# Performance work log

Hardware: AMD Instinct MI355X
Metric: run time of the kernel (lower is better)

## Reference

```python
import jax, jax.numpy as jnp
import numpy as np

B, D, O, E, H, K = 4096, 1024, 1024, 8, 4096, 2


def setup_inputs() -> dict:
    key = jax.random.key(0)
    ks = jax.random.split(key, 5)
    scale_g = 1.0 / np.sqrt(D)
    scale_1 = 1.0 / np.sqrt(D)
    scale_2 = 1.0 / np.sqrt(H)
    return {
        "x": jax.random.normal(ks[0], (B, D), jnp.float32),
        "gate_w": jax.random.normal(ks[1], (D, E), jnp.float32) * scale_g,
        "gate_b": jnp.zeros((E,), jnp.float32),
        "w1": jax.random.normal(ks[2], (E, D, H), jnp.float32) * scale_1,
        "b1": jnp.zeros((E, H), jnp.float32),
        "w2": jax.random.normal(ks[3], (E, H, O), jnp.float32) * scale_2,
        "b2": jnp.zeros((E, O), jnp.float32),
    }


def reference(x, gate_w, gate_b, w1, b1, w2, b2):
    # Router: top-k logits, softmax over the k selected logits only
    logits = x @ gate_w + gate_b                      # [B, E]
    top_vals, top_idx = jax.lax.top_k(logits, K)      # [B, K]
    routing_w = jax.nn.softmax(top_vals, axis=-1)     # [B, K]

    # Dense all-expert MLP (grouped GEMM), then gather the k selected outputs
    h = jax.nn.relu(jnp.einsum("bd,edh->beh", x, w1) + b1)  # [B, E, H]
    y = jnp.einsum("beh,eho->beo", h, w2) + b2              # [B, E, O]
    sel = jnp.take_along_axis(y, top_idx[:, :, None], axis=1)  # [B, K, O]
    return jnp.sum(routing_w[:, :, None] * sel, axis=1)        # [B, O]
```

## Files before the change

### kernel.cpp

```cpp
#include <hip/hip_runtime.h>
#include <stdint.h>

typedef short bf16x8 __attribute__((ext_vector_type(8)));
typedef float f32x4  __attribute__((ext_vector_type(4)));

constexpr int BT = 4096;
constexpr int DD = 1024;
constexpr int OO = 1024;
constexpr int EE = 8;
constexpr int HH = 4096;
constexpr int SLOTS = 2 * BT;

constexpr int BM = 128, BN = 128, BK = 32;
constexpr int A_USH = BM * BK;
constexpr int SLOT_USH = (BM + BN) * BK;
constexpr int MAXT = 72;
constexpr int G1_BLKS = 32 * MAXT;
constexpr int G2_BLKS = 8 * MAXT * 2;

__device__ __forceinline__ unsigned short f2bf(float f) {
  unsigned u = __float_as_uint(f);
  u += 0x7fffu + ((u >> 16) & 1u);
  return (unsigned short)(u >> 16);
}

__device__ __forceinline__ void glds16(const unsigned short* g, unsigned short* l) {
  __builtin_amdgcn_global_load_lds(
      (const __attribute__((address_space(1))) void*)g,
      (__attribute__((address_space(3))) void*)l, 16, 0, 0);
}

__device__ __forceinline__ void cvt_body(const float* __restrict__ src,
                                         unsigned short* __restrict__ dst,
                                         int R, int C, int e, int r0, int c0, int t,
                                         unsigned short (*tile)[66]) {
  const float* s = src + (size_t)e * R * C;
  unsigned short* d = dst + (size_t)e * R * C;
#pragma unroll
  for (int p = 0; p < 4; ++p) {
    int ch = p * 256 + t;
    int rr = ch >> 4, cc = (ch & 15) << 2;
    float4 v = *(const float4*)&s[(size_t)(r0 + rr) * C + c0 + cc];
    unsigned lo = (unsigned)f2bf(v.x) | ((unsigned)f2bf(v.y) << 16);
    unsigned hi = (unsigned)f2bf(v.z) | ((unsigned)f2bf(v.w) << 16);
    *(uint2*)&tile[rr][cc] = make_uint2(lo, hi);
  }
  __syncthreads();
#pragma unroll
  for (int p = 0; p < 4; ++p) {
    int ch = p * 256 + t;
    int cc = ch >> 4, rr = (ch & 15) << 2;
    unsigned short v0 = tile[rr + 0][cc];
    unsigned short v1 = tile[rr + 1][cc];
    unsigned short v2 = tile[rr + 2][cc];
    unsigned short v3 = tile[rr + 3][cc];
    unsigned lo = (unsigned)v0 | ((unsigned)v1 << 16);
    unsigned hi = (unsigned)v2 | ((unsigned)v3 << 16);
    *(uint2*)&d[(size_t)(c0 + cc) * R + r0 + rr] = make_uint2(lo, hi);
  }
}

__global__ __launch_bounds__(256) void fusedA_k(const float* __restrict__ x,
                                                const float* __restrict__ gw,
                                                const float* __restrict__ gb,
                                                const float* __restrict__ w1,
                                                unsigned short* __restrict__ xb,
                                                int* __restrict__ cnt,
                                                int* __restrict__ list,
                                                float* __restrict__ rw,
                                                unsigned short* __restrict__ w1t) {
  __shared__ unsigned short tile[64][66];
  int bid = blockIdx.x;
  if (bid >= 1024) {
    int idx = bid - 1024;
    int e = idx >> 10, rem = idx & 1023;
    int r0 = (rem & 15) << 6, c0 = (rem >> 4) << 6;
    cvt_body(w1, w1t, DD, HH, e, r0, c0, threadIdx.x, tile);
    return;
  }
  int wave = threadIdx.x >> 6, lane = threadIdx.x & 63;
  int b = bid * 4 + wave;
  const float* xrow = x + (size_t)b * DD;
  float acc[8];
#pragma unroll
  for (int e = 0; e < 8; ++e) acc[e] = 0.f;
#pragma unroll
  for (int i = 0; i < 4; ++i) {
    int d0 = i * 256 + lane * 4;
    float4 v = *(const float4*)&xrow[d0];
    unsigned lo = (unsigned)f2bf(v.x) | ((unsigned)f2bf(v.y) << 16);
    unsigned hi = (unsigned)f2bf(v.z) | ((unsigned)f2bf(v.w) << 16);
    *(uint2*)&xb[(size_t)b * DD + d0] = make_uint2(lo, hi);
    const float* g0 = &gw[(size_t)d0 * 8];
    float fv[4] = {v.x, v.y, v.z, v.w};
#pragma unroll
    for (int q = 0; q < 4; ++q) {
      float4 ga = *(const float4*)&g0[q * 8];
      float4 gc = *(const float4*)&g0[q * 8 + 4];
      acc[0] += fv[q] * ga.x; acc[1] += fv[q] * ga.y;
      acc[2] += fv[q] * ga.z; acc[3] += fv[q] * ga.w;
      acc[4] += fv[q] * gc.x; acc[5] += fv[q] * gc.y;
      acc[6] += fv[q] * gc.z; acc[7] += fv[q] * gc.w;
    }
  }
#pragma unroll
  for (int off = 32; off > 0; off >>= 1) {
#pragma unroll
    for (int e = 0; e < 8; ++e) acc[e] += __shfl_down(acc[e], off);
  }
  if (lane == 0) {
    float v[8];
#pragma unroll
    for (int e = 0; e < 8; ++e) v[e] = acc[e] + gb[e];
    int i0 = 0;
#pragma unroll
    for (int e = 1; e < 8; ++e) if (v[e] > v[i0]) i0 = e;
    int i1 = (i0 == 0) ? 1 : 0;
#pragma unroll
    for (int e = 0; e < 8; ++e) if (e != i0 && v[e] > v[i1]) i1 = e;
    float e1 = __expf(v[i1] - v[i0]);
    float inv = 1.0f / (1.0f + e1);
    int p0 = atomicAdd(&cnt[i0], 1);
    list[i0 * BT + p0] = 2 * b;     rw[2 * b]     = inv;
    int p1 = atomicAdd(&cnt[i1], 1);
    list[i1 * BT + p1] = 2 * b + 1; rw[2 * b + 1] = e1 * inv;
  }
}

__global__ void tilemap_k(const int* __restrict__ cnt, int* __restrict__ tmap,
                          int* __restrict__ ntiles) {
  if (threadIdx.x == 0 && blockIdx.x == 0) {
    int t = 0, basewalk = 0;
    for (int e = 0; e < EE; ++e) {
      int c = cnt[e];
      for (int m0 = 0; m0 < c; m0 += BM) {
        tmap[4 * t] = e; tmap[4 * t + 1] = m0; tmap[4 * t + 2] = basewalk + m0; ++t;
      }
      basewalk += c;
    }
    *ntiles = t;
  }
}

__global__ __launch_bounds__(256) void cvt_t_k(const float* __restrict__ src,
                                               unsigned short* __restrict__ dst,
                                               int R, int C) {
  __shared__ unsigned short tile[64][66];
  cvt_body(src, dst, R, C, blockIdx.z, blockIdx.x << 6, blockIdx.y << 6,
           threadIdx.x, tile);
}

__global__ __launch_bounds__(256, 3) void fusedB_k(const unsigned short* __restrict__ xb,
                                                   const unsigned short* __restrict__ w1t,
                                                   const float* __restrict__ b1,
                                                   const int* __restrict__ cnt,
                                                   const int* __restrict__ list,
                                                   const int* __restrict__ tmap,
                                                   const int* __restrict__ ntiles,
                                                   unsigned short* __restrict__ hc,
                                                   const float* __restrict__ w2,
                                                   unsigned short* __restrict__ w2t) {
  __shared__ __align__(16) unsigned short lds[3 * SLOT_USH];
  __shared__ int slotbuf[BM];
  int bid = blockIdx.x;
  if (bid >= G1_BLKS) {
    int idx = bid - G1_BLKS;
    int e = idx >> 10, rem = idx & 1023;
    int r0 = (rem & 63) << 6, c0 = (rem >> 6) << 6;
    cvt_body(w2, w2t, HH, OO, e, r0, c0, threadIdx.x,
             (unsigned short (*)[66])lds);
    return;
  }
  int q = bid & 7, kk = bid >> 3;
  int n0 = (kk & 31) * BN;
  int ti = (kk >> 5) * 8 + q;
  if (ti >= *ntiles) return;
  int e = tmap[4 * ti], m0 = tmap[4 * ti + 1], base = tmap[4 * ti + 2];
  int cnt_e = cnt[e];

  int t = threadIdx.x;
  if (t < BM) {
    int r = m0 + t;
    slotbuf[t] = list[e * BT + (r < cnt_e ? r : 0)];
  }
  __syncthreads();

  int w = t >> 6, l = t & 63, lm = l & 15, lq = l >> 4;
  int wm = (w >> 1) * 64, wn = (w & 1) * 64;

  const unsigned short* aS[2];
  const unsigned short* bS[2];
  int dA[2], dB[2];
#pragma unroll
  for (int j = 0; j < 2; ++j) {
    int row = w * 32 + j * 16 + (l >> 2);
    int sch = ((l & 3) ^ ((row >> 1) & 3)) * 8;
    aS[j] = xb + (size_t)(slotbuf[row] >> 1) * DD + sch;
    bS[j] = w1t + (size_t)e * HH * DD + (size_t)(n0 + row) * DD + sch;
    dA[j] = w * 1024 + j * 512;
    dB[j] = A_USH + w * 1024 + j * 512;
  }

  int xs = (lq ^ ((lm >> 1) & 3)) * 8;
  int afo[4], bfo[4];
#pragma unroll
  for (int mi = 0; mi < 4; ++mi) afo[mi] = (wm + mi * 16 + lm) * BK + xs;
#pragma unroll
  for (int ni = 0; ni < 4; ++ni) bfo[ni] = A_USH + (wn + ni * 16 + lm) * BK + xs;

  f32x4 acc[4][4];
#pragma unroll
  for (int mi = 0; mi < 4; ++mi)
#pragma unroll
    for (int ni = 0; ni < 4; ++ni) acc[mi][ni] = f32x4{0.f, 0.f, 0.f, 0.f};

  constexpr int NT = DD / BK;

#pragma unroll
  for (int p = 0; p < 2; ++p) {
    unsigned short* Lb = lds + p * SLOT_USH;
    glds16(aS[0] + p * BK, Lb + dA[0]);
    glds16(aS[1] + p * BK, Lb + dA[1]);
    glds16(bS[0] + p * BK, Lb + dB[0]);
    glds16(bS[1] + p * BK, Lb + dB[1]);
  }
  asm volatile("s_waitcnt vmcnt(4)" ::: "memory");
  __builtin_amdgcn_s_barrier();
  asm volatile("" ::: "memory");

  int sc = 0, ss = 2;
  for (int tt = 0; tt < NT; ++tt) {
    {
      int ts = tt + 2;
      int ko = (ts < NT ? ts : NT - 1) * BK;
      unsigned short* Lb = lds + ss * SLOT_USH;
      glds16(aS[0] + ko, Lb + dA[0]);
      glds16(aS[1] + ko, Lb + dA[1]);
      glds16(bS[0] + ko, Lb + dB[0]);
      glds16(bS[1] + ko, Lb + dB[1]);
    }
    const unsigned short* Lc = lds + sc * SLOT_USH;
    bf16x8 af[4], bf[4];
#pragma unroll
    for (int mi = 0; mi < 4; ++mi) af[mi] = *(const bf16x8*)&Lc[afo[mi]];
#pragma unroll
    for (int ni = 0; ni < 4; ++ni) bf[ni] = *(const bf16x8*)&Lc[bfo[ni]];
    __builtin_amdgcn_s_setprio(1);
#pragma unroll
    for (int mi = 0; mi < 4; ++mi)
#pragma unroll
      for (int ni = 0; ni < 4; ++ni)
        acc[mi][ni] = __builtin_amdgcn_mfma_f32_16x16x32_bf16(af[mi], bf[ni], acc[mi][ni], 0, 0, 0);
    __builtin_amdgcn_s_setprio(0);
    asm volatile("s_waitcnt vmcnt(4)" ::: "memory");
    __builtin_amdgcn_s_barrier();
    asm volatile("" ::: "memory");
    if (++sc == 3) sc = 0;
    if (++ss == 3) ss = 0;
  }

  asm volatile("s_waitcnt vmcnt(0)" ::: "memory");
  __builtin_amdgcn_s_barrier();
  asm volatile("" ::: "memory");
  unsigned short* cb = lds + w * 4096;
  float bias[4];
#pragma unroll
  for (int ni = 0; ni < 4; ++ni) bias[ni] = b1[e * HH + n0 + wn + ni * 16 + lm];
#pragma unroll
  for (int mi = 0; mi < 4; ++mi)
#pragma unroll
    for (int ni = 0; ni < 4; ++ni)
#pragma unroll
      for (int r = 0; r < 4; ++r)
        cb[(mi * 16 + lq * 4 + r) * 64 + ni * 16 + lm] =
            f2bf(fmaxf(acc[mi][ni][r] + bias[ni], 0.0f));
  asm volatile("s_waitcnt lgkmcnt(0)" ::: "memory");
#pragma unroll
  for (int it = 0; it < 8; ++it) {
    int rr = it * 8 + (l >> 3), chk = l & 7;
    int grow = wm + rr;
    if (m0 + grow < cnt_e) {
      uint4 v = *(const uint4*)&cb[rr * 64 + chk * 8];
      *(uint4*)&hc[(size_t)(base + grow) * HH + n0 + wn + chk * 8] = v;
    }
  }
}

__global__ __launch_bounds__(256, 3) void gemm2_k(const unsigned short* __restrict__ hc,
                                                  const unsigned short* __restrict__ w2t,
                                                  const float* __restrict__ b2,
                                                  const int* __restrict__ cnt,
                                                  const int* __restrict__ list,
                                                  const int* __restrict__ tmap,
                                                  const int* __restrict__ ntiles,
                                                  const float* __restrict__ rw,
                                                  float* __restrict__ ybuf,
                                                  float* __restrict__ out) {
  int q = blockIdx.x & 7, kk = blockIdx.x >> 3;
  int n0 = (kk & 7) * BN;
  int mz = (kk >> 3) * 8 + q;
  int z = mz / MAXT;
  int ti = mz % MAXT;
  if (ti >= *ntiles) return;
  int e = tmap[4 * ti], m0 = tmap[4 * ti + 1], base = tmap[4 * ti + 2];
  int cnt_e = cnt[e];
  int kb0 = z * (HH / 2);
  constexpr int NT = (HH / 2) / BK;

  __shared__ __align__(16) unsigned short lds[3 * SLOT_USH];
  __shared__ int slotbuf[BM];
  __shared__ float rwbuf[BM];

  int t = threadIdx.x;
  if (t < BM) {
    int r = m0 + t;
    int s_ = list[e * BT + (r < cnt_e ? r : 0)];
    slotbuf[t] = s_;
    rwbuf[t] = rw[s_];
  }
  __syncthreads();

  int w = t >> 6, l = t & 63, lm = l & 15, lq = l >> 4;
  int wm = (w >> 1) * 64, wn = (w & 1) * 64;

  const unsigned short* aS[2];
  const unsigned short* bS[2];
  int dA[2], dB[2];
#pragma unroll
  for (int j = 0; j < 2; ++j) {
    int row = w * 32 + j * 16 + (l >> 2);
    int sch = ((l & 3) ^ ((row >> 1) & 3)) * 8;
    int gr = base + row; if (gr > SLOTS - 1) gr = SLOTS - 1;
    aS[j] = hc + (size_t)gr * HH + kb0 + sch;
    bS[j] = w2t + (size_t)e * OO * HH + (size_t)(n0 + row) * HH + kb0 + sch;
    dA[j] = w * 1024 + j * 512;
    dB[j] = A_USH + w * 1024 + j * 512;
  }

  int xs = (lq ^ ((lm >> 1) & 3)) * 8;
  int afo[4], bfo[4];
#pragma unroll
  for (int mi = 0; mi < 4; ++mi) afo[mi] = (wm + mi * 16 + lm) * BK + xs;
#pragma unroll
  for (int ni = 0; ni < 4; ++ni) bfo[ni] = A_USH + (wn + ni * 16 + lm) * BK + xs;

  f32x4 acc[4][4];
#pragma unroll
  for (int mi = 0; mi < 4; ++mi)
#pragma unroll
    for (int ni = 0; ni < 4; ++ni) acc[mi][ni] = f32x4{0.f, 0.f, 0.f, 0.f};

#pragma unroll
  for (int p = 0; p < 2; ++p) {
    unsigned short* Lb = lds + p * SLOT_USH;
    glds16(aS[0] + p * BK, Lb + dA[0]);
    glds16(aS[1] + p * BK, Lb + dA[1]);
    glds16(bS[0] + p * BK, Lb + dB[0]);
    glds16(bS[1] + p * BK, Lb + dB[1]);
  }
  asm volatile("s_waitcnt vmcnt(4)" ::: "memory");
  __builtin_amdgcn_s_barrier();
  asm volatile("" ::: "memory");

  int sc = 0, ss = 2;
  for (int tt = 0; tt < NT; ++tt) {
    {
      int ts = tt + 2;
      int ko = (ts < NT ? ts : NT - 1) * BK;
      unsigned short* Lb = lds + ss * SLOT_USH;
      glds16(aS[0] + ko, Lb + dA[0]);
      glds16(aS[1] + ko, Lb + dA[1]);
      glds16(bS[0] + ko, Lb + dB[0]);
      glds16(bS[1] + ko, Lb + dB[1]);
    }
    const unsigned short* Lc = lds + sc * SLOT_USH;
    bf16x8 af[4], bf[4];
#pragma unroll
    for (int mi = 0; mi < 4; ++mi) af[mi] = *(const bf16x8*)&Lc[afo[mi]];
#pragma unroll
    for (int ni = 0; ni < 4; ++ni) bf[ni] = *(const bf16x8*)&Lc[bfo[ni]];
    __builtin_amdgcn_s_setprio(1);
#pragma unroll
    for (int mi = 0; mi < 4; ++mi)
#pragma unroll
      for (int ni = 0; ni < 4; ++ni)
        acc[mi][ni] = __builtin_amdgcn_mfma_f32_16x16x32_bf16(af[mi], bf[ni], acc[mi][ni], 0, 0, 0);
    __builtin_amdgcn_s_setprio(0);
    asm volatile("s_waitcnt vmcnt(4)" ::: "memory");
    __builtin_amdgcn_s_barrier();
    asm volatile("" ::: "memory");
    if (++sc == 3) sc = 0;
    if (++ss == 3) ss = 0;
  }
  asm volatile("s_waitcnt vmcnt(0)" ::: "memory");

  bool addb = (z == 0);
  size_t ybase = (size_t)z * SLOTS;
#pragma unroll
  for (int ni = 0; ni < 4; ++ni) {
    int ncol = n0 + wn + ni * 16 + lm;
    float bias = addb ? b2[e * OO + ncol] : 0.0f;
#pragma unroll
    for (int mi = 0; mi < 4; ++mi)
#pragma unroll
      for (int r = 0; r < 4; ++r) {
        int lrow = wm + mi * 16 + lq * 4 + r;
        if (m0 + lrow < cnt_e) {
          float v = (acc[mi][ni][r] + bias) * rwbuf[lrow];
          int slot = slotbuf[lrow];
          if (ybuf) ybuf[(ybase + slot) * OO + ncol] = v;
          else      atomicAdd(&out[(size_t)(slot >> 1) * OO + ncol], v);
        }
      }
  }
}

__global__ __launch_bounds__(256) void combine_k(const float* __restrict__ y,
                                                 float* __restrict__ out, int nz) {
  int i = blockIdx.x * 256 + threadIdx.x;
  int b = i >> 8, c = i & 255;
  f32x4 acc = {0.f, 0.f, 0.f, 0.f};
  for (int z = 0; z < nz; ++z) {
#pragma unroll
    for (int k = 0; k < 2; ++k) {
      const float4 v = *(const float4*)&y[((size_t)z * SLOTS + 2 * b + k) * OO + c * 4];
      acc[0] += v.x; acc[1] += v.y; acc[2] += v.z; acc[3] += v.w;
    }
  }
  *(f32x4*)&out[(size_t)b * OO + c * 4] = acc;
}

extern "C" void kernel_launch(void* const* d_in, const int* in_sizes, int n_in,
                              void* d_out, int out_size, void* d_ws, size_t ws_size,
                              hipStream_t stream) {
  const float* x  = (const float*)d_in[0];
  const float* gw = (const float*)d_in[1];
  const float* gb = (const float*)d_in[2];
  const float* w1 = (const float*)d_in[3];
  const float* b1 = (const float*)d_in[4];
  const float* w2 = (const float*)d_in[5];
  const float* b2 = (const float*)d_in[6];
  float* out = (float*)d_out;
  char* ws = (char*)d_ws;

  int*            cnt    = (int*)(ws);
  int*            ntiles = (int*)(ws + 64);
  int*            tmap   = (int*)(ws + 128);
  float*          rw     = (float*)(ws + 4096);
  int*            list   = (int*)(ws + (64u << 10));
  unsigned short* xb     = (unsigned short*)(ws + (1u  << 20));
  unsigned short* w1t    = (unsigned short*)(ws + (9u  << 20));

  bool roomy = ws_size >= (201u << 20);
  hipMemsetAsync(cnt, 0, 64, stream);

  if (roomy) {
    unsigned short* w2t = (unsigned short*)(ws + (73u  << 20));
    unsigned short* hc  = (unsigned short*)(ws + (137u << 20));
    float*          ybuf = (float*)(ws + (9u << 20));

    fusedA_k<<<1024 + 8192, 256, 0, stream>>>(x, gw, gb, w1, xb, cnt, list, rw, w1t);
    tilemap_k<<<1, 64, 0, stream>>>(cnt, tmap, ntiles);
    fusedB_k<<<G1_BLKS + 8192, 256, 0, stream>>>(xb, w1t, b1, cnt, list, tmap, ntiles,
                                                 hc, w2, w2t);
    gemm2_k<<<G2_BLKS, 256, 0, stream>>>(hc, w2t, b2, cnt, list, tmap,
                                         ntiles, rw, ybuf, out);
    combine_k<<<BT * OO / 1024, 256, 0, stream>>>(ybuf, out, 2);
  } else {
    if (ws_size < (137u << 20)) return;
    unsigned short* w2t = w1t;
    unsigned short* hc  = (unsigned short*)(ws + (73u << 20));
    hipMemsetAsync(out, 0, (size_t)BT * OO * sizeof(float), stream);
    fusedA_k<<<1024 + 8192, 256, 0, stream>>>(x, gw, gb, w1, xb, cnt, list, rw, w1t);
    tilemap_k<<<1, 64, 0, stream>>>(cnt, tmap, ntiles);
    fusedB_k<<<G1_BLKS, 256, 0, stream>>>(xb, w1t, b1, cnt, list, tmap, ntiles,
                                          hc, w2, w2t);
    cvt_t_k<<<dim3(HH / 64, OO / 64, EE), 256, 0, stream>>>(w2, w2t, HH, OO);
    gemm2_k<<<G2_BLKS, 256, 0, stream>>>(hc, w2t, b2, cnt, list, tmap,
                                         ntiles, rw, nullptr, out);
  }
}
```

Baseline: 654.6 us.

## Pin each expert's tiles to one XCD via per-expert tile start offsets

Both grouped GEMM kernels now map blockIdx low bits to the expert index, using per-expert tile start offsets written by tilemap_k. Before, tiles were laid out linearly across all experts. Because blocks are dispatched round-robin across XCDs, each XCD should mostly stream a single expert's weights, which is meant to improve L2 reuse of w1t and w2t. The grid is sized for the worst case of 32 tiles per expert, so many blocks exit at once. It also risks XCD load imbalance when routing is skewed toward some experts.

```diff
diff --git a/kernel.cpp b/kernel.cpp
--- a/kernel.cpp
+++ b/kernel.cpp
@@ -14,9 +14,9 @@
 constexpr int BM = 128, BN = 128, BK = 32;
 constexpr int A_USH = BM * BK;
 constexpr int SLOT_USH = (BM + BN) * BK;
-constexpr int MAXT = 72;
-constexpr int G1_BLKS = 32 * MAXT;
-constexpr int G2_BLKS = 8 * MAXT * 2;
+constexpr int MTS = 32;
+constexpr int G1_BLKS = 8 * 32 * MTS;
+constexpr int G2_BLKS = 8 * 2 * 8 * MTS;
 
 __device__ __forceinline__ unsigned short f2bf(float f) {
   unsigned u = __float_as_uint(f);
@@ -128,16 +128,18 @@
 }
 
 __global__ void tilemap_k(const int* __restrict__ cnt, int* __restrict__ tmap,
-                          int* __restrict__ ntiles) {
+                          int* __restrict__ ntiles, int* __restrict__ tstart) {
   if (threadIdx.x == 0 && blockIdx.x == 0) {
     int t = 0, basewalk = 0;
     for (int e = 0; e < EE; ++e) {
+      tstart[e] = t;
       int c = cnt[e];
       for (int m0 = 0; m0 < c; m0 += BM) {
         tmap[4 * t] = e; tmap[4 * t + 1] = m0; tmap[4 * t + 2] = basewalk + m0; ++t;
       }
       basewalk += c;
     }
+    tstart[EE] = t;
     *ntiles = t;
   }
 }
@@ -156,7 +158,7 @@
                                                    const int* __restrict__ cnt,
                                                    const int* __restrict__ list,
                                                    const int* __restrict__ tmap,
-                                                   const int* __restrict__ ntiles,
+                                                   const int* __restrict__ tstart,
                                                    unsigned short* __restrict__ hc,
                                                    const float* __restrict__ w2,
                                                    unsigned short* __restrict__ w2t) {
@@ -171,17 +173,19 @@
              (unsigned short (*)[66])lds);
     return;
   }
-  int q = bid & 7, kk = bid >> 3;
-  int n0 = (kk & 31) * BN;
-  int ti = (kk >> 5) * 8 + q;
-  if (ti >= *ntiles) return;
+  int q = bid & 7, r = bid >> 3;
+  int mts = r & (MTS - 1), nt = r >> 5;
+  int tc0 = tstart[q];
+  if (tc0 + mts >= tstart[q + 1]) return;
+  int ti = tc0 + mts;
   int e = tmap[4 * ti], m0 = tmap[4 * ti + 1], base = tmap[4 * ti + 2];
   int cnt_e = cnt[e];
+  int n0 = nt * BN;
 
   int t = threadIdx.x;
   if (t < BM) {
-    int r = m0 + t;
-    slotbuf[t] = list[e * BT + (r < cnt_e ? r : 0)];
+    int rr = m0 + t;
+    slotbuf[t] = list[e * BT + (rr < cnt_e ? rr : 0)];
   }
   __syncthreads();
 
@@ -271,9 +275,9 @@
 #pragma unroll
     for (int ni = 0; ni < 4; ++ni)
 #pragma unroll
-      for (int r = 0; r < 4; ++r)
-        cb[(mi * 16 + lq * 4 + r) * 64 + ni * 16 + lm] =
-            f2bf(fmaxf(acc[mi][ni][r] + bias[ni], 0.0f));
+      for (int rr = 0; rr < 4; ++rr)
+        cb[(mi * 16 + lq * 4 + rr) * 64 + ni * 16 + lm] =
+            f2bf(fmaxf(acc[mi][ni][rr] + bias[ni], 0.0f));
   asm volatile("s_waitcnt lgkmcnt(0)" ::: "memory");
 #pragma unroll
   for (int it = 0; it < 8; ++it) {
@@ -292,18 +296,19 @@
                                                   const int* __restrict__ cnt,
                                                   const int* __restrict__ list,
                                                   const int* __restrict__ tmap,
-                                                  const int* __restrict__ ntiles,
+                                                  const int* __restrict__ tstart,
                                                   const float* __restrict__ rw,
                                                   float* __restrict__ ybuf,
                                                   float* __restrict__ out) {
-  int q = blockIdx.x & 7, kk = blockIdx.x >> 3;
-  int n0 = (kk & 7) * BN;
-  int mz = (kk >> 3) * 8 + q;
-  int z = mz / MAXT;
-  int ti = mz % MAXT;
-  if (ti >= *ntiles) return;
+  int q = blockIdx.x & 7, r = blockIdx.x >> 3;
+  int z = r >> 8, s = r & 255;
+  int mts = s & (MTS - 1), nt = s >> 5;
+  int tc0 = tstart[q];
+  if (tc0 + mts >= tstart[q + 1]) return;
+  int ti = tc0 + mts;
   int e = tmap[4 * ti], m0 = tmap[4 * ti + 1], base = tmap[4 * ti + 2];
   int cnt_e = cnt[e];
+  int n0 = nt * BN;
   int kb0 = z * (HH / 2);
   constexpr int NT = (HH / 2) / BK;
 
@@ -313,8 +318,8 @@
 
   int t = threadIdx.x;
   if (t < BM) {
-    int r = m0 + t;
-    int s_ = list[e * BT + (r < cnt_e ? r : 0)];
+    int rr = m0 + t;
+    int s_ = list[e * BT + (rr < cnt_e ? rr : 0)];
     slotbuf[t] = s_;
     rwbuf[t] = rw[s_];
   }
@@ -403,10 +408,10 @@
 #pragma unroll
     for (int mi = 0; mi < 4; ++mi)
 #pragma unroll
-      for (int r = 0; r < 4; ++r) {
-        int lrow = wm + mi * 16 + lq * 4 + r;
+      for (int rr = 0; rr < 4; ++rr) {
+        int lrow = wm + mi * 16 + lq * 4 + rr;
         if (m0 + lrow < cnt_e) {
-          float v = (acc[mi][ni][r] + bias) * rwbuf[lrow];
+          float v = (acc[mi][ni][rr] + bias) * rwbuf[lrow];
           int slot = slotbuf[lrow];
           if (ybuf) ybuf[(ybase + slot) * OO + ncol] = v;
           else      atomicAdd(&out[(size_t)(slot >> 1) * OO + ncol], v);
@@ -446,6 +451,7 @@
   int*            cnt    = (int*)(ws);
   int*            ntiles = (int*)(ws + 64);
   int*            tmap   = (int*)(ws + 128);
+  int*            tstart = (int*)(ws + 2560);
   float*          rw     = (float*)(ws + 4096);
   int*            list   = (int*)(ws + (64u << 10));
   unsigned short* xb     = (unsigned short*)(ws + (1u  << 20));
@@ -460,11 +466,11 @@
     float*          ybuf = (float*)(ws + (9u << 20));
 
     fusedA_k<<<1024 + 8192, 256, 0, stream>>>(x, gw, gb, w1, xb, cnt, list, rw, w1t);
-    tilemap_k<<<1, 64, 0, stream>>>(cnt, tmap, ntiles);
-    fusedB_k<<<G1_BLKS + 8192, 256, 0, stream>>>(xb, w1t, b1, cnt, list, tmap, ntiles,
+    tilemap_k<<<1, 64, 0, stream>>>(cnt, tmap, ntiles, tstart);
+    fusedB_k<<<G1_BLKS + 8192, 256, 0, stream>>>(xb, w1t, b1, cnt, list, tmap, tstart,
                                                  hc, w2, w2t);
     gemm2_k<<<G2_BLKS, 256, 0, stream>>>(hc, w2t, b2, cnt, list, tmap,
-                                         ntiles, rw, ybuf, out);
+                                         tstart, rw, ybuf, out);
     combine_k<<<BT * OO / 1024, 256, 0, stream>>>(ybuf, out, 2);
   } else {
     if (ws_size < (137u << 20)) return;
@@ -472,11 +478,11 @@
     unsigned short* hc  = (unsigned short*)(ws + (73u << 20));
     hipMemsetAsync(out, 0, (size_t)BT * OO * sizeof(float), stream);
     fusedA_k<<<1024 + 8192, 256, 0, stream>>>(x, gw, gb, w1, xb, cnt, list, rw, w1t);
-    tilemap_k<<<1, 64, 0, stream>>>(cnt, tmap, ntiles);
-    fusedB_k<<<G1_BLKS, 256, 0, stream>>>(xb, w1t, b1, cnt, list, tmap, ntiles,
+    tilemap_k<<<1, 64, 0, stream>>>(cnt, tmap, ntiles, tstart);
+    fusedB_k<<<G1_BLKS, 256, 0, stream>>>(xb, w1t, b1, cnt, list, tmap, tstart,
                                           hc, w2, w2t);
     cvt_t_k<<<dim3(HH / 64, OO / 64, EE), 256, 0, stream>>>(w2, w2t, HH, OO);
     gemm2_k<<<G2_BLKS, 256, 0, stream>>>(hc, w2t, b2, cnt, list, tmap,
-                                         ntiles, rw, nullptr, out);
-  }
-}
+                                         tstart, rw, nullptr, out);
+  }
+}
```

Result: no change. 642.8 us (-1.8%).
